# Performance work log

Measured on AMD Instinct MI355X. Metric: run time of the kernel, lower is better.

Reference implementation:

```python
import jax, jax.numpy as jnp
import numpy as np

IMAGE_W = 1024
IMAGE_H = 1024
STRIDES = (8, 16, 32, 64, 128)
TOP_N = 1000
MIN_SCORE = 0.05
NMS_THR = 0.6
MAX_DET = 100
NEG = -1e9  # sentinel for suppressed scores


def _positions(stride):
    # Faithful to repo: shifts_x indexed by feature_h, shifts_y by feature_w,
    # grid built [hf, wf, 2] = [shift_x_i, shift_y_j], then permute(1,0,2).
    hf, wf = IMAGE_H // stride, IMAGE_W // stride
    sx = (jnp.arange(hf, dtype=jnp.float32) + 0.5) * stride
    sy = (jnp.arange(wf, dtype=jnp.float32) + 0.5) * stride
    pos = jnp.stack(jnp.meshgrid(sx, sy, indexing='ij'), axis=-1)  # [hf, wf, 2]
    return jnp.transpose(pos, (1, 0, 2)).reshape(-1, 2)  # [hf*wf, 2]


def _filter_level(cls_h, reg_h, ctr_h, pos):
    B, C = cls_h.shape[0], cls_h.shape[-1]
    cls_h = jax.nn.sigmoid(cls_h).reshape(B, -1, C)
    reg_h = jnp.exp(reg_h).reshape(B, -1, 4)
    ctr_h = jax.nn.sigmoid(ctr_h).reshape(B, -1)
    scores = jnp.max(cls_h, axis=-1)
    classes = jnp.argmax(cls_h, axis=-1).astype(jnp.int32)
    scores = jnp.sqrt(scores * ctr_h)
    N = scores.shape[1]
    if N >= TOP_N:
        scores, idx = jax.lax.top_k(scores, TOP_N)  # sorted descending, like torch.topk
        classes = jnp.take_along_axis(classes, idx, axis=1)
        reg_h = jnp.take_along_axis(reg_h, idx[..., None], axis=1)
        posb = pos[idx]  # [B, TOP_N, 2]
    else:
        posb = jnp.broadcast_to(pos[None], (B, N, 2))
    return scores, classes, reg_h, posb


def _snap(reg, pos):
    # reg: [B, N, 4] (l,t,r,b), pos: [B, N, 2]
    b = jnp.concatenate([pos - reg[:, :, 0:2], pos + reg[:, :, 2:4]], axis=-1)
    b = b.astype(jnp.int32)  # torch .int() truncation
    b = jnp.stack([
        jnp.maximum(b[..., 0], 0),
        jnp.maximum(b[..., 1], 0),
        jnp.minimum(b[..., 2], IMAGE_W - 1),
        jnp.minimum(b[..., 3], IMAGE_H - 1),
    ], axis=-1)
    return b.astype(jnp.float32)


def _nms_image(scores, classes, boxes):
    # scores [N], classes [N] int32, boxes [N,4] float (already snapped to int grid)
    s = jnp.where(scores > MIN_SCORE, scores, NEG)
    x1, y1, x2, y2 = boxes[:, 0], boxes[:, 1], boxes[:, 2], boxes[:, 3]
    areas = (x2 - x1) * (y2 - y1)
    out_s = -jnp.ones((MAX_DET,), jnp.float32)
    out_c = -jnp.ones((MAX_DET,), jnp.float32)
    out_b = -jnp.ones((MAX_DET, 4), jnp.float32)

    def body(i, st):
        s, os_, oc, ob = st
        idx = jnp.argmax(s)            # highest remaining score -> sorted keep order
        ok = s[idx] > MIN_SCORE        # any un-suppressed valid candidate left?
        bb = boxes[idx]
        iw = jnp.clip(jnp.minimum(x2, bb[2]) - jnp.maximum(x1, bb[0]), 0.0)
        ih = jnp.clip(jnp.minimum(y2, bb[3]) - jnp.maximum(y1, bb[1]), 0.0)
        inter = iw * ih
        iou = inter / (areas + areas[idx] - inter + 1e-12)
        s = jnp.where((iou > NMS_THR) & ok, NEG, s)
        s = s.at[idx].set(NEG)
        os_ = os_.at[i].set(jnp.where(ok, scores[idx], -1.0))
        oc = oc.at[i].set(jnp.where(ok, classes[idx].astype(jnp.float32), -1.0))
        ob = ob.at[i].set(jnp.where(ok, bb, -jnp.ones((4,), jnp.float32)))
        return (s, os_, oc, ob)

    _, os_, oc, ob = jax.lax.fori_loop(0, MAX_DET, body, (s, out_s, out_c, out_b))
    return os_, oc, ob


def _decode(cls_heads, reg_heads, ctr_heads):
    sc_l, cl_l, rg_l, ps_l = [], [], [], []
    for c, r, t, st in zip(cls_heads, reg_heads, ctr_heads, STRIDES):
        sc, cl, rg, ps = _filter_level(c, r, t, _positions(st))
        sc_l.append(sc); cl_l.append(cl); rg_l.append(rg); ps_l.append(ps)
    scores = jnp.concatenate(sc_l, axis=1)
    classes = jnp.concatenate(cl_l, axis=1)
    regs = jnp.concatenate(rg_l, axis=1)
    poss = jnp.concatenate(ps_l, axis=1)
    boxes = _snap(regs, poss)
    return jax.vmap(_nms_image)(scores, classes, boxes)


def setup_inputs() -> dict:
    key = jax.random.key(0)
    ks = jax.random.split(key, 15)
    B, C = 8, 80
    sizes = [IMAGE_H // s for s in STRIDES]
    inp = {}
    for i, hw in enumerate(sizes):
        inp[f'cls{i}'] = jax.random.normal(ks[i], (B, hw, hw, C), dtype=jnp.float32)
        # +3 so exp(reg) gives realistic ~20px extents
        inp[f'reg{i}'] = jax.random.normal(ks[5 + i], (B, hw, hw, 4), dtype=jnp.float32) + 3.0
        inp[f'ctr{i}'] = jax.random.normal(ks[10 + i], (B, hw, hw, 1), dtype=jnp.float32)
    return inp


def reference(cls0, cls1, cls2, cls3, cls4,
              reg0, reg1, reg2, reg3, reg4,
              ctr0, ctr1, ctr2, ctr3, ctr4):
    cls_heads = [cls0, cls1, cls2, cls3, cls4]
    reg_heads = [reg0, reg1, reg2, reg3, reg4]
    ctr_heads = [ctr0, ctr1, ctr2, ctr3, ctr4]
    batch_scores, batch_classes, batch_boxes = _decode(cls_heads, reg_heads, ctr_heads)
    return batch_scores, batch_classes, batch_boxes
```

## Files before the change

### kernel.cpp

```cpp
#include <hip/hip_runtime.h>

#define NPOS 21824
#define NCK  1088
#define MINS 0.05f
#define BT   1024
#define NW   (BT/64)

struct Ptrs { const float* cls[5]; const float* reg[5]; const float* ctr[5]; };

__device__ __forceinline__ float sigf(float x){ return 1.0f/(1.0f+expf(-x)); }

__global__ __launch_bounds__(256) void k_score(Ptrs P, float* scoreAll, int* clsAll,
                                               float4* boxAll)
{
    int img  = blockIdx.y;
    int blk  = blockIdx.x;
    int tid  = threadIdx.x;
    int posb = tid >> 2;
    int l    = tid & 3;
    int p    = blk*64 + posb;
    int lvl, base, lw, stride;
    if (blk < 256)      { lvl=0; base=0;     lw=7; stride=8;   }
    else if (blk < 320) { lvl=1; base=16384; lw=6; stride=16;  }
    else if (blk < 336) { lvl=2; base=20480; lw=5; stride=32;  }
    else if (blk < 340) { lvl=3; base=21504; lw=4; stride=64;  }
    else                { lvl=4; base=21760; lw=3; stride=128; }
    int pl = p - base;
    int h = pl >> lw, w = pl & ((1<<lw)-1);
    long long lidx = (long long)img*(1<<(2*lw)) + pl;

    const float4* c4 = (const float4*)(P.cls[lvl] + lidx*80);
    float mx = -3.4e38f; int mi = 0;
#pragma unroll
    for (int j = 0; j < 5; ++j) {
        int k = j*4 + l;
        float4 v = c4[k];
        int cb = k*4;
        if (v.x > mx){mx=v.x; mi=cb;}
        if (v.y > mx){mx=v.y; mi=cb+1;}
        if (v.z > mx){mx=v.z; mi=cb+2;}
        if (v.w > mx){mx=v.w; mi=cb+3;}
    }
#pragma unroll
    for (int d = 1; d < 4; d <<= 1) {
        float omx = __shfl_xor(mx, d);
        int   omi = __shfl_xor(mi, d);
        if (omx > mx || (omx == mx && omi < mi)) { mx = omx; mi = omi; }
    }
    if (l == 0) {
        float ct = P.ctr[lvl][lidx];
        float sc = sqrtf(sigf(mx)*sigf(ct));
        float4 rg = ((const float4*)P.reg[lvl])[lidx];
        float x = (w + 0.5f)*(float)stride;
        float y = (h + 0.5f)*(float)stride;
        int ix1 = (int)(x - expf(rg.x));
        int iy1 = (int)(y - expf(rg.y));
        int ix2 = (int)(x + expf(rg.z));
        int iy2 = (int)(y + expf(rg.w));
        ix1 = max(ix1,0); iy1 = max(iy1,0);
        ix2 = min(ix2,1023); iy2 = min(iy2,1023);
        int o = img*NPOS + p;
        scoreAll[o] = sc;
        clsAll[o]   = mi;
        boxAll[o]   = make_float4((float)ix1,(float)iy1,(float)ix2,(float)iy2);
    }
}

__device__ void radix24(const unsigned int* vals, int N, int K,
                        int* histA, int* histB, int* wsum,
                        unsigned int* shPref, int* shK, int tid)
{
    for (int i = tid; i < N; i += BT)
        atomicAdd(&histA[vals[i] >> 19], 1);
    __syncthreads();
    {
        int lo = tid*2;
        int ls = histA[lo] + histA[lo+1];
        int lane = tid & 63, wv = tid >> 6;
        int v = ls;
#pragma unroll
        for (int off = 1; off < 64; off <<= 1) {
            int o = __shfl_down(v, off);
            if (lane + off < 64) v += o;
        }
        if (lane == 0) wsum[wv] = v;
        __syncthreads();
        int add = 0;
        for (int q = wv + 1; q < NW; ++q) add += wsum[q];
        int mine = v + add;
        int above = mine - ls;
        if (above < K && mine >= K) {
            if (above + histA[lo+1] >= K) { *shPref = (unsigned)(lo+1) << 19; *shK = K - above; }
            else { *shPref = (unsigned)lo << 19; *shK = K - above - histA[lo+1]; }
        }
        __syncthreads();
    }
    unsigned int pref = *shPref;
    int K2 = *shK;
    for (int i = tid; i < N; i += BT) {
        unsigned int b = vals[i];
        if ((b >> 19) == (pref >> 19)) atomicAdd(&histB[(b >> 8) & 2047], 1);
    }
    __syncthreads();
    {
        int lo = tid*2;
        int ls = histB[lo] + histB[lo+1];
        int lane = tid & 63, wv = tid >> 6;
        int v = ls;
#pragma unroll
        for (int off = 1; off < 64; off <<= 1) {
            int o = __shfl_down(v, off);
            if (lane + off < 64) v += o;
        }
        if (lane == 0) wsum[wv] = v;
        __syncthreads();
        int add = 0;
        for (int q = wv + 1; q < NW; ++q) add += wsum[q];
        int mine = v + add;
        int above = mine - ls;
        if (above < K2 && mine >= K2) {
            if (above + histB[lo+1] >= K2) { *shPref = pref | ((unsigned)(lo+1) << 8); *shK = K2 - above; }
            else { *shPref = pref | ((unsigned)lo << 8); *shK = K2 - above - histB[lo+1]; }
        }
        __syncthreads();
    }
}

__global__ __launch_bounds__(BT) void k_thresh(const float* scoreAll,
                                               unsigned long long* cKeyG)
{
    __shared__ int histA[2048], histB[2048], wsum[NW];
    __shared__ unsigned int shPref;
    __shared__ int shK, tick, eqn;
    __shared__ int eq[1024];
    int il = blockIdx.x, tid = threadIdx.x;

    if (il >= 24) {
        int img = il - 24;
        const unsigned int* gs = (const unsigned int*)scoreAll + (long long)img*NPOS;
        unsigned long long* gk = cKeyG + (long long)img*NCK;
        for (int i = tid; i < 320; i += BT) {
            int p = 21504 + i;
            gk[768 + i] = ((unsigned long long)gs[p] << 16) | (unsigned)(65535 - p);
        }
        return;
    }
    int img = il / 3, lvl = il % 3;
    const int baseA[3] = {0, 16384, 20480};
    const int NlA[3]   = {16384, 4096, 1024};
    int base = baseA[lvl], Nl = NlA[lvl];
    const unsigned int* gs = (const unsigned int*)scoreAll + (long long)img*NPOS + base;
    unsigned long long* gk = cKeyG + (long long)img*NCK + lvl*256;

    for (int i = tid; i < 2048; i += BT) { histA[i] = 0; histB[i] = 0; }
    if (tid == 0) { tick = 0; eqn = 0; }
    __syncthreads();
    radix24(gs, Nl, 256, histA, histB, wsum, &shPref, &shK, tid);
    unsigned int kth = shPref >> 8;
    int need = shK;
    for (int i = tid; i < Nl; i += BT) {
        unsigned int b = gs[i], hb = b >> 8;
        if (hb > kth) {
            int t = atomicAdd(&tick, 1);
            int p = base + i;
            gk[t] = ((unsigned long long)b << 16) | (unsigned)(65535 - p);
        } else if (hb == kth) {
            int t = atomicAdd(&eqn, 1);
            if (t < 1024) eq[t] = i;
        }
    }
    __syncthreads();
    int m = eqn, nG = tick;
    if (m <= 1024) {
        for (int q = tid; q < m; q += BT) {
            int iq = eq[q];
            unsigned int bq = gs[iq];
            int r = 0;
            for (int j = 0; j < m; ++j) {
                int ij = eq[j];
                unsigned int bj = gs[ij];
                r += (bj > bq) || (bj == bq && ij < iq);
            }
            if (r < need) {
                int p = base + iq;
                gk[nG + r] = ((unsigned long long)bq << 16) | (unsigned)(65535 - p);
            }
        }
    } else if (tid == 0) {
        unsigned long long last = ~0ULL;
        for (int c = 0; c < need; ++c) {
            unsigned long long best = 0;
            for (int i = 0; i < Nl; ++i) {
                unsigned int b = gs[i];
                if ((b >> 8) == kth) {
                    unsigned long long k = ((unsigned long long)b << 16)
                                         | (unsigned)(65535 - (base + i));
                    if (k < last && k > best) best = k;
                }
            }
            gk[nG + c] = best; last = best;
        }
    }
}

__global__ __launch_bounds__(BT) void k_nms2(const unsigned long long* cKeyG,
                                             const float4* boxAll, const int* clsAll,
                                             float* out)
{
    __shared__ unsigned long long cand[NCK];
    __shared__ unsigned int cbits[NCK];
    __shared__ int histA[2048], histB[2048], wsum[NW];
    __shared__ unsigned int shPref;
    __shared__ int shK, tick, eqn;
    __shared__ int eq[256];
    __shared__ unsigned long long sel[256];
    __shared__ unsigned long long sorted[256];
    __shared__ float4 sBox[256];
    __shared__ float  sCls[256];
    __shared__ __align__(16) unsigned long long sRow[256][4];
    __shared__ int accIdx[100];
    __shared__ int shNaM, shNaT;

    int img = blockIdx.x, tid = threadIdx.x;
    const float4* gBox = boxAll + (long long)img*NPOS;
    const int*    gCls = clsAll + (long long)img*NPOS;
    const unsigned long long* gKey = cKeyG + (long long)img*NCK;

    float* outS = out + img*100;
    float* outC = out + 800 + img*100;
    float* outB = out + 1600 + img*400;

    for (int i = tid; i < NCK; i += BT) {
        unsigned long long k = gKey[i];
        cand[i]  = k;
        cbits[i] = (unsigned int)(k >> 16);
    }
    for (int i = tid; i < 2048; i += BT) { histA[i] = 0; histB[i] = 0; }
    if (tid == 0) { tick = 0; eqn = 0; }
    __syncthreads();

    radix24(cbits, NCK, 256, histA, histB, wsum, &shPref, &shK, tid);
    unsigned int kth2 = shPref >> 8;
    int need2 = shK;
    for (int i = tid; i < NCK; i += BT) {
        unsigned int hb = cbits[i] >> 8;
        if (hb > kth2)       { int t = atomicAdd(&tick, 1); sel[t] = cand[i]; }
        else if (hb == kth2) { int t = atomicAdd(&eqn, 1); if (t < 256) eq[t] = i; }
    }
    __syncthreads();
    int m2 = eqn, nG2 = tick;
    if (m2 <= 256) {
        for (int q = tid; q < m2; q += BT) {
            unsigned long long kq = cand[eq[q]];
            int r = 0;
            for (int j = 0; j < m2; ++j) r += (cand[eq[j]] > kq);
            if (r < need2) sel[nG2 + r] = kq;
        }
    } else if (tid == 0) {
        unsigned long long last = ~0ULL;
        for (int c = 0; c < need2; ++c) {
            unsigned long long best = 0;
            for (int i = 0; i < NCK; ++i) {
                unsigned long long k = cand[i];
                if ((unsigned int)(k >> 24) == kth2 && k < last && k > best) best = k;
            }
            sel[nG2 + c] = best; last = best;
        }
    }
    __syncthreads();

    if (tid < 256) {
        unsigned long long k = sel[tid];
        int r = 0;
        for (int j = 0; j < 256; ++j) r += (sel[j] > k);
        sorted[r] = k;
    }
    __syncthreads();
    if (tid < 256) {
        int p = 65535 - (int)(sorted[tid] & 0xFFFF);
        sBox[tid] = gBox[p];
        sCls[tid] = (float)gCls[p];
    }

    float myScore = 0.f;
    if (tid < 256) myScore = __uint_as_float((unsigned int)(sorted[tid] >> 16));
    int nValid = __syncthreads_count(myScore > MINS ? 1 : 0);

    {
        int row = tid & 255, qq = tid >> 8;
        float4 bi = sBox[row];
        float  ai = (bi.z-bi.x)*(bi.w-bi.y);
        unsigned long long mv = 0;
#pragma unroll 8
        for (int jj = 0; jj < 64; ++jj) {
            int j = qq*64 + jj;
            float4 bj = sBox[j];
            float aj = (bj.z-bj.x)*(bj.w-bj.y);
            float iw = fmaxf(fminf(bj.z,bi.z)-fmaxf(bj.x,bi.x),0.f);
            float ih = fmaxf(fminf(bj.w,bi.w)-fmaxf(bj.y,bi.y),0.f);
            float in_ = iw*ih;
            bool s = (j > row) && (in_/(aj+ai-in_+1e-12f) > 0.6f);
            mv |= ((unsigned long long)s) << jj;
        }
        sRow[row][qq] = mv;
    }
    __syncthreads();

    if (tid == 0) {
        int na = 0;
        unsigned long long r0=0, r1=0, r2=0, r3=0;
#define FCOS_WBLK(RW, IB)                                                  \
        {                                                                  \
            int hi = nValid < ((IB)+1)*64 ? nValid : ((IB)+1)*64;          \
            for (int i = (IB)*64; i < hi && na < 100; ++i) {               \
                if ((RW >> (i - (IB)*64)) & 1ull) continue;                \
                accIdx[na++] = i;                                          \
                const ulonglong2* rp = (const ulonglong2*)sRow[i];         \
                ulonglong2 ra = rp[0], rb = rp[1];                         \
                r0 |= ra.x; r1 |= ra.y; r2 |= rb.x; r3 |= rb.y;            \
            }                                                              \
        }
        FCOS_WBLK(r0,0) FCOS_WBLK(r1,1) FCOS_WBLK(r2,2) FCOS_WBLK(r3,3)
#undef FCOS_WBLK
        shNaM = na; shNaT = na;
    }

    if (tid < 64) {
        int lane = tid;
        int naM = shNaM;
        if (naM < 100 && nValid == 256) {
            int na = naM;
            float4 aB0 = make_float4(0,0,0,0), aB1 = make_float4(0,0,0,0);
            float  aA0 = 0.f, aA1 = 0.f;
            if (lane < na)      { aB0 = sBox[accIdx[lane]];
                                  aA0 = (aB0.z-aB0.x)*(aB0.w-aB0.y); }
            if (lane + 64 < na) { aB1 = sBox[accIdx[lane+64]];
                                  aA1 = (aB1.z-aB1.x)*(aB1.w-aB1.y); }
            unsigned long long thr = sorted[255];
            for (int j = lane; j < NCK; j += 64)
                if (cand[j] >= thr) cand[j] = 0ULL;
            __threadfence_block();
            while (na < 100) {
                unsigned long long bk = 0; int bidx = -1;
                for (int j = lane; j < NCK; j += 64) {
                    unsigned long long v = cand[j];
                    if (v > bk) { bk = v; bidx = j; }
                }
#pragma unroll
                for (int off = 32; off > 0; off >>= 1) {
                    unsigned long long ov = __shfl_down(bk, off);
                    int oi = __shfl_down(bidx, off);
                    if (ov > bk) { bk = ov; bidx = oi; }
                }
                bk = __shfl(bk, 0); bidx = __shfl(bidx, 0);
                if (bk == 0ULL) break;
                float sc = __uint_as_float((unsigned int)(bk >> 16));
                if (!(sc > MINS)) break;
                int p = 65535 - (int)(bk & 0xFFFF);
                float4 bb2 = gBox[p];
                float ba = (bb2.z-bb2.x)*(bb2.w-bb2.y);
                bool sup = false;
                if (lane < na) {
                    float iw = fmaxf(fminf(bb2.z,aB0.z)-fmaxf(bb2.x,aB0.x),0.f);
                    float ih = fmaxf(fminf(bb2.w,aB0.w)-fmaxf(bb2.y,aB0.y),0.f);
                    float in_ = iw*ih;
                    sup = in_/(ba+aA0-in_+1e-12f) > 0.6f;
                }
                if (lane + 64 < na) {
                    float iw = fmaxf(fminf(bb2.z,aB1.z)-fmaxf(bb2.x,aB1.x),0.f);
                    float ih = fmaxf(fminf(bb2.w,aB1.w)-fmaxf(bb2.y,aB1.y),0.f);
                    float in_ = iw*ih;
                    sup = sup || (in_/(ba+aA1-in_+1e-12f) > 0.6f);
                }
                if (__ballot(sup) == 0ULL) {
                    if (lane == 0) {
                        outS[na] = sc;
                        outC[na] = (float)gCls[p];
                        outB[4*na+0]=bb2.x; outB[4*na+1]=bb2.y;
                        outB[4*na+2]=bb2.z; outB[4*na+3]=bb2.w;
                    }
                    if (lane == (na & 63)) {
                        if (na < 64) { aB0 = bb2; aA0 = ba; }
                        else         { aB1 = bb2; aA1 = ba; }
                    }
                    ++na;
                }
                if (lane == 0) cand[bidx] = 0ULL;
                __threadfence_block();
            }
            if (lane == 0) shNaT = na;
        }
    }
    __syncthreads();

    {
        int naM = shNaM, naT = shNaT;
        if (tid < 100) {
            if (tid < naM) {
                int r = accIdx[tid];
                unsigned long long k = sorted[r];
                float4 b = sBox[r];
                outS[tid] = __uint_as_float((unsigned int)(k >> 16));
                outC[tid] = sCls[r];
                outB[4*tid+0]=b.x; outB[4*tid+1]=b.y;
                outB[4*tid+2]=b.z; outB[4*tid+3]=b.w;
            } else if (tid >= naT) {
                outS[tid] = -1.f; outC[tid] = -1.f;
                outB[4*tid+0]=-1.f; outB[4*tid+1]=-1.f;
                outB[4*tid+2]=-1.f; outB[4*tid+3]=-1.f;
            }
        }
    }
}

extern "C" void kernel_launch(void* const* d_in, const int* in_sizes, int n_in,
                              void* d_out, int out_size, void* d_ws, size_t ws_size,
                              hipStream_t stream) {
    Ptrs P;
    bool interleaved = (in_sizes[1] == 8 * 128 * 128 * 4);
    for (int i = 0; i < 5; ++i) {
        if (interleaved) {
            P.cls[i] = (const float*)d_in[3*i];
            P.reg[i] = (const float*)d_in[3*i + 1];
            P.ctr[i] = (const float*)d_in[3*i + 2];
        } else {
            P.cls[i] = (const float*)d_in[i];
            P.reg[i] = (const float*)d_in[5 + i];
            P.ctr[i] = (const float*)d_in[10 + i];
        }
    }

    char* wbase = (char*)d_ws;
    size_t off = 0;
    auto alloc = [&](size_t bytes) -> void* {
        void* r = wbase + off;
        off += (bytes + 255) & ~(size_t)255;
        return r;
    };
    float*              scoreAll = (float*)alloc((size_t)8 * NPOS * 4);
    int*                clsAll   = (int*)alloc((size_t)8 * NPOS * 4);
    float4*             boxAll   = (float4*)alloc((size_t)8 * NPOS * 16);
    unsigned long long* cKeyG    = (unsigned long long*)alloc((size_t)8 * NCK * 8);

    dim3 gA(341, 8);
    k_score <<<gA, 256, 0, stream>>>(P, scoreAll, clsAll, boxAll);
    k_thresh<<<32, BT, 0, stream>>>(scoreAll, cKeyG);
    k_nms2  <<<8, BT, 0, stream>>>(cKeyG, boxAll, clsAll, (float*)d_out);
}
```

Measured before the change: 162.6 us.

## Fuse threshold selection into NMS kernel with single global radix select

Removes the separate per-level threshold kernel and its global candidate-key buffer. Each image's block now radix-selects the top 256 keys directly over all 21824 scores. The serial fallback NMS, used when fewer than 100 boxes survive, becomes a block-wide scan over all scores with __syncthreads_count voting, instead of a single wavefront over the 1088-entry candidate list. This saves a kernel launch and an intermediate global round-trip. In exchange, each of only 8 blocks does a larger selection pass, and the fallback loop costs more per iteration.

Result: no change. 159.7 us (-1.8%).

```diff
diff --git a/kernel.cpp b/kernel.cpp
--- a/kernel.cpp
+++ b/kernel.cpp
@@ -1,7 +1,6 @@
 #include <hip/hip_runtime.h>
 
 #define NPOS 21824
-#define NCK  1088
 #define MINS 0.05f
 #define BT   1024
 #define NW   (BT/64)
@@ -9,6 +8,10 @@
 struct Ptrs { const float* cls[5]; const float* reg[5]; const float* ctr[5]; };
 
 __device__ __forceinline__ float sigf(float x){ return 1.0f/(1.0f+expf(-x)); }
+
+__device__ __forceinline__ unsigned long long mkkey(unsigned int b, int p){
+    return ((unsigned long long)b << 16) | (unsigned)(65535 - p);
+}
 
 __global__ __launch_bounds__(256) void k_score(Ptrs P, float* scoreAll, int* clsAll,
                                                float4* boxAll)
@@ -126,145 +129,66 @@
     }
 }
 
-__global__ __launch_bounds__(BT) void k_thresh(const float* scoreAll,
-                                               unsigned long long* cKeyG)
+__global__ __launch_bounds__(BT) void k_nms(const float* scoreAll,
+                                            const float4* boxAll, const int* clsAll,
+                                            float* out)
 {
     __shared__ int histA[2048], histB[2048], wsum[NW];
     __shared__ unsigned int shPref;
     __shared__ int shK, tick, eqn;
-    __shared__ int eq[1024];
-    int il = blockIdx.x, tid = threadIdx.x;
-
-    if (il >= 24) {
-        int img = il - 24;
-        const unsigned int* gs = (const unsigned int*)scoreAll + (long long)img*NPOS;
-        unsigned long long* gk = cKeyG + (long long)img*NCK;
-        for (int i = tid; i < 320; i += BT) {
-            int p = 21504 + i;
-            gk[768 + i] = ((unsigned long long)gs[p] << 16) | (unsigned)(65535 - p);
-        }
-        return;
-    }
-    int img = il / 3, lvl = il % 3;
-    const int baseA[3] = {0, 16384, 20480};
-    const int NlA[3]   = {16384, 4096, 1024};
-    int base = baseA[lvl], Nl = NlA[lvl];
-    const unsigned int* gs = (const unsigned int*)scoreAll + (long long)img*NPOS + base;
-    unsigned long long* gk = cKeyG + (long long)img*NCK + lvl*256;
-
-    for (int i = tid; i < 2048; i += BT) { histA[i] = 0; histB[i] = 0; }
-    if (tid == 0) { tick = 0; eqn = 0; }
-    __syncthreads();
-    radix24(gs, Nl, 256, histA, histB, wsum, &shPref, &shK, tid);
-    unsigned int kth = shPref >> 8;
-    int need = shK;
-    for (int i = tid; i < Nl; i += BT) {
-        unsigned int b = gs[i], hb = b >> 8;
-        if (hb > kth) {
-            int t = atomicAdd(&tick, 1);
-            int p = base + i;
-            gk[t] = ((unsigned long long)b << 16) | (unsigned)(65535 - p);
-        } else if (hb == kth) {
-            int t = atomicAdd(&eqn, 1);
-            if (t < 1024) eq[t] = i;
-        }
-    }
-    __syncthreads();
-    int m = eqn, nG = tick;
-    if (m <= 1024) {
-        for (int q = tid; q < m; q += BT) {
-            int iq = eq[q];
-            unsigned int bq = gs[iq];
-            int r = 0;
-            for (int j = 0; j < m; ++j) {
-                int ij = eq[j];
-                unsigned int bj = gs[ij];
-                r += (bj > bq) || (bj == bq && ij < iq);
-            }
-            if (r < need) {
-                int p = base + iq;
-                gk[nG + r] = ((unsigned long long)bq << 16) | (unsigned)(65535 - p);
-            }
-        }
-    } else if (tid == 0) {
-        unsigned long long last = ~0ULL;
-        for (int c = 0; c < need; ++c) {
-            unsigned long long best = 0;
-            for (int i = 0; i < Nl; ++i) {
-                unsigned int b = gs[i];
-                if ((b >> 8) == kth) {
-                    unsigned long long k = ((unsigned long long)b << 16)
-                                         | (unsigned)(65535 - (base + i));
-                    if (k < last && k > best) best = k;
-                }
-            }
-            gk[nG + c] = best; last = best;
-        }
-    }
-}
-
-__global__ __launch_bounds__(BT) void k_nms2(const unsigned long long* cKeyG,
-                                             const float4* boxAll, const int* clsAll,
-                                             float* out)
-{
-    __shared__ unsigned long long cand[NCK];
-    __shared__ unsigned int cbits[NCK];
-    __shared__ int histA[2048], histB[2048], wsum[NW];
-    __shared__ unsigned int shPref;
-    __shared__ int shK, tick, eqn;
-    __shared__ int eq[256];
+    __shared__ unsigned long long eqKey[1024];
     __shared__ unsigned long long sel[256];
     __shared__ unsigned long long sorted[256];
     __shared__ float4 sBox[256];
     __shared__ float  sCls[256];
     __shared__ __align__(16) unsigned long long sRow[256][4];
     __shared__ int accIdx[100];
-    __shared__ int shNaM, shNaT;
+    __shared__ float4 accBox[100];
+    __shared__ int shNaM, shNa;
+    __shared__ unsigned long long shLast;
 
     int img = blockIdx.x, tid = threadIdx.x;
+    const unsigned int* gs = (const unsigned int*)scoreAll + (long long)img*NPOS;
     const float4* gBox = boxAll + (long long)img*NPOS;
     const int*    gCls = clsAll + (long long)img*NPOS;
-    const unsigned long long* gKey = cKeyG + (long long)img*NCK;
 
     float* outS = out + img*100;
     float* outC = out + 800 + img*100;
     float* outB = out + 1600 + img*400;
 
-    for (int i = tid; i < NCK; i += BT) {
-        unsigned long long k = gKey[i];
-        cand[i]  = k;
-        cbits[i] = (unsigned int)(k >> 16);
-    }
     for (int i = tid; i < 2048; i += BT) { histA[i] = 0; histB[i] = 0; }
     if (tid == 0) { tick = 0; eqn = 0; }
     __syncthreads();
 
-    radix24(cbits, NCK, 256, histA, histB, wsum, &shPref, &shK, tid);
-    unsigned int kth2 = shPref >> 8;
-    int need2 = shK;
-    for (int i = tid; i < NCK; i += BT) {
-        unsigned int hb = cbits[i] >> 8;
-        if (hb > kth2)       { int t = atomicAdd(&tick, 1); sel[t] = cand[i]; }
-        else if (hb == kth2) { int t = atomicAdd(&eqn, 1); if (t < 256) eq[t] = i; }
-    }
-    __syncthreads();
-    int m2 = eqn, nG2 = tick;
-    if (m2 <= 256) {
-        for (int q = tid; q < m2; q += BT) {
-            unsigned long long kq = cand[eq[q]];
+    radix24(gs, NPOS, 256, histA, histB, wsum, &shPref, &shK, tid);
+    unsigned int kth = shPref >> 8;
+    int need = shK;
+    for (int i = tid; i < NPOS; i += BT) {
+        unsigned int b = gs[i], hb = b >> 8;
+        if (hb > kth)       { int t = atomicAdd(&tick, 1); sel[t] = mkkey(b, i); }
+        else if (hb == kth) { int t = atomicAdd(&eqn, 1); if (t < 1024) eqKey[t] = mkkey(b, i); }
+    }
+    __syncthreads();
+    int m = eqn, nG = tick;
+    if (m <= 1024) {
+        for (int q = tid; q < m; q += BT) {
+            unsigned long long kq = eqKey[q];
             int r = 0;
-            for (int j = 0; j < m2; ++j) r += (cand[eq[j]] > kq);
-            if (r < need2) sel[nG2 + r] = kq;
+            for (int j = 0; j < m; ++j) r += (eqKey[j] > kq);
+            if (r < need) sel[nG + r] = kq;
         }
     } else if (tid == 0) {
         unsigned long long last = ~0ULL;
-        for (int c = 0; c < need2; ++c) {
+        for (int c = 0; c < need; ++c) {
             unsigned long long best = 0;
-            for (int i = 0; i < NCK; ++i) {
-                unsigned long long k = cand[i];
-                if ((unsigned int)(k >> 24) == kth2 && k < last && k > best) best = k;
-            }
-            sel[nG2 + c] = best; last = best;
+            for (int i = 0; i < NPOS; ++i) {
+                unsigned int b = gs[i];
+                if ((b >> 8) == kth) {
+                    unsigned long long k2 = mkkey(b, i);
+                    if (k2 < last && k2 > best) best = k2;
+                }
+            }
+            sel[nG + c] = best; last = best;
         }
     }
     __syncthreads();
@@ -322,81 +246,75 @@
         }
         FCOS_WBLK(r0,0) FCOS_WBLK(r1,1) FCOS_WBLK(r2,2) FCOS_WBLK(r3,3)
 #undef FCOS_WBLK
-        shNaM = na; shNaT = na;
-    }
-
-    if (tid < 64) {
-        int lane = tid;
-        int naM = shNaM;
-        if (naM < 100 && nValid == 256) {
-            int na = naM;
-            float4 aB0 = make_float4(0,0,0,0), aB1 = make_float4(0,0,0,0);
-            float  aA0 = 0.f, aA1 = 0.f;
-            if (lane < na)      { aB0 = sBox[accIdx[lane]];
-                                  aA0 = (aB0.z-aB0.x)*(aB0.w-aB0.y); }
-            if (lane + 64 < na) { aB1 = sBox[accIdx[lane+64]];
-                                  aA1 = (aB1.z-aB1.x)*(aB1.w-aB1.y); }
-            unsigned long long thr = sorted[255];
-            for (int j = lane; j < NCK; j += 64)
-                if (cand[j] >= thr) cand[j] = 0ULL;
-            __threadfence_block();
-            while (na < 100) {
-                unsigned long long bk = 0; int bidx = -1;
-                for (int j = lane; j < NCK; j += 64) {
-                    unsigned long long v = cand[j];
-                    if (v > bk) { bk = v; bidx = j; }
+        shNaM = na; shNa = na;
+    }
+    __syncthreads();
+
+    int naM = shNaM;
+    if (naM < 100 && nValid == 256) {
+        if (tid < naM) accBox[tid] = sBox[accIdx[tid]];
+        if (tid == 0) shLast = sorted[255];
+        __syncthreads();
+        while (true) {
+            if (shNa >= 100) break;
+            unsigned long long last = shLast;
+            unsigned long long bk = 0;
+            for (int i = tid; i < NPOS; i += BT) {
+                unsigned long long k2 = mkkey(gs[i], i);
+                if (k2 < last && k2 > bk) bk = k2;
+            }
+#pragma unroll
+            for (int off = 32; off > 0; off >>= 1) {
+                unsigned long long o = __shfl_down(bk, off);
+                if (o > bk) bk = o;
+            }
+            int lane = tid & 63, wv = tid >> 6;
+            if (lane == 0) eqKey[wv] = bk;
+            __syncthreads();
+            if (tid == 0) {
+                unsigned long long best = 0;
+                for (int q = 0; q < NW; ++q) if (eqKey[q] > best) best = eqKey[q];
+                shLast = best;
+            }
+            __syncthreads();
+            unsigned long long ck = shLast;
+            if (ck == 0ULL) break;
+            float sc = __uint_as_float((unsigned int)(ck >> 16));
+            if (!(sc > MINS)) break;
+            int p = 65535 - (int)(ck & 0xFFFF);
+            float4 bb = gBox[p];
+            float ba = (bb.z-bb.x)*(bb.w-bb.y);
+            int na = shNa;
+            bool mySup = false;
+            if (tid < na) {
+                float4 ab = accBox[tid];
+                float aa = (ab.z-ab.x)*(ab.w-ab.y);
+                float iw = fmaxf(fminf(bb.z,ab.z)-fmaxf(bb.x,ab.x),0.f);
+                float ih = fmaxf(fminf(bb.w,ab.w)-fmaxf(bb.y,ab.y),0.f);
+                float in_ = iw*ih;
+                mySup = in_/(ba+aa-in_+1e-12f) > 0.6f;
+            }
+            int supCnt = __syncthreads_count(mySup);
+            if (supCnt == 0) {
+                if (tid == 0) {
+                    int na2 = shNa;
+                    outS[na2] = sc;
+                    outC[na2] = (float)gCls[p];
+                    outB[4*na2+0]=bb.x; outB[4*na2+1]=bb.y;
+                    outB[4*na2+2]=bb.z; outB[4*na2+3]=bb.w;
+                    accBox[na2] = bb;
+                    shNa = na2 + 1;
                 }
-#pragma unroll
-                for (int off = 32; off > 0; off >>= 1) {
-                    unsigned long long ov = __shfl_down(bk, off);
-                    int oi = __shfl_down(bidx, off);
-                    if (ov > bk) { bk = ov; bidx = oi; }
-                }
-                bk = __shfl(bk, 0); bidx = __shfl(bidx, 0);
-                if (bk == 0ULL) break;
-                float sc = __uint_as_float((unsigned int)(bk >> 16));
-                if (!(sc > MINS)) break;
-                int p = 65535 - (int)(bk & 0xFFFF);
-                float4 bb2 = gBox[p];
-                float ba = (bb2.z-bb2.x)*(bb2.w-bb2.y);
-                bool sup = false;
-                if (lane < na) {
-                    float iw = fmaxf(fminf(bb2.z,aB0.z)-fmaxf(bb2.x,aB0.x),0.f);
-                    float ih = fmaxf(fminf(bb2.w,aB0.w)-fmaxf(bb2.y,aB0.y),0.f);
-                    float in_ = iw*ih;
-                    sup = in_/(ba+aA0-in_+1e-12f) > 0.6f;
-                }
-                if (lane + 64 < na) {
-                    float iw = fmaxf(fminf(bb2.z,aB1.z)-fmaxf(bb2.x,aB1.x),0.f);
-                    float ih = fmaxf(fminf(bb2.w,aB1.w)-fmaxf(bb2.y,aB1.y),0.f);
-                    float in_ = iw*ih;
-                    sup = sup || (in_/(ba+aA1-in_+1e-12f) > 0.6f);
-                }
-                if (__ballot(sup) == 0ULL) {
-                    if (lane == 0) {
-                        outS[na] = sc;
-                        outC[na] = (float)gCls[p];
-                        outB[4*na+0]=bb2.x; outB[4*na+1]=bb2.y;
-                        outB[4*na+2]=bb2.z; outB[4*na+3]=bb2.w;
-                    }
-                    if (lane == (na & 63)) {
-                        if (na < 64) { aB0 = bb2; aA0 = ba; }
-                        else         { aB1 = bb2; aA1 = ba; }
-                    }
-                    ++na;
-                }
-                if (lane == 0) cand[bidx] = 0ULL;
-                __threadfence_block();
-            }
-            if (lane == 0) shNaT = na;
+            }
+            __syncthreads();
         }
     }
     __syncthreads();
 
     {
-        int naM = shNaM, naT = shNaT;
+        int naM2 = shNaM, naT = shNa;
         if (tid < 100) {
-            if (tid < naM) {
+            if (tid < naM2) {
                 int r = accIdx[tid];
                 unsigned long long k = sorted[r];
                 float4 b = sBox[r];
@@ -437,13 +355,11 @@
         off += (bytes + 255) & ~(size_t)255;
         return r;
     };
-    float*              scoreAll = (float*)alloc((size_t)8 * NPOS * 4);
-    int*                clsAll   = (int*)alloc((size_t)8 * NPOS * 4);
-    float4*             boxAll   = (float4*)alloc((size_t)8 * NPOS * 16);
-    unsigned long long* cKeyG    = (unsigned long long*)alloc((size_t)8 * NCK * 8);
+    float*  scoreAll = (float*)alloc((size_t)8 * NPOS * 4);
+    int*    clsAll   = (int*)alloc((size_t)8 * NPOS * 4);
+    float4* boxAll   = (float4*)alloc((size_t)8 * NPOS * 16);
 
     dim3 gA(341, 8);
     k_score <<<gA, 256, 0, stream>>>(P, scoreAll, clsAll, boxAll);
-    k_thresh<<<32, BT, 0, stream>>>(scoreAll, cKeyG);
-    k_nms2  <<<8, BT, 0, stream>>>(cKeyG, boxAll, clsAll, (float*)d_out);
-}
+    k_nms   <<<8, BT, 0, stream>>>(scoreAll, boxAll, clsAll, (float*)d_out);
+}
```
